# Kernel optimization log

Measured on AMD Instinct MI355X. Metric: run time of the kernel, lower is better.

The kernel has to match this reference:

```python
import jax, jax.numpy as jnp
import numpy as np


def _resize1d(x, axis, out_size):
    """Bilinear resize along one axis, align_corners=False (PyTorch semantics,
    no antialias). x: any shape; interpolates along `axis` to out_size."""
    in_size = x.shape[axis]
    src = (jnp.arange(out_size, dtype=jnp.float32) + 0.5) * (in_size / out_size) - 0.5
    src = jnp.clip(src, 0.0, in_size - 1)
    i0 = jnp.floor(src).astype(jnp.int32)
    i1 = jnp.minimum(i0 + 1, in_size - 1)
    w = (src - i0.astype(jnp.float32))
    x0 = jnp.take(x, i0, axis=axis)
    x1 = jnp.take(x, i1, axis=axis)
    shape = [1] * x.ndim
    shape[axis] = out_size
    w = w.reshape(shape)
    return x0 * (1.0 - w) + x1 * w


def bilinear_resize(x, h_out, w_out):
    """x: (..., H, W) -> (..., h_out, w_out), bilinear align_corners=False."""
    x = _resize1d(x, x.ndim - 2, h_out)
    x = _resize1d(x, x.ndim - 1, w_out)
    return x


def _deform_corr_single(f1, f2, off):
    """f1, f2: (C, H, W); off: (2, H, W) with off[0]=dx, off[1]=dy.
    Bilinearly sample f2 at (x+dx, y+dy) with zero padding outside, then
    channel dot-product with f1 -> (H, W)."""
    C, H, W = f1.shape
    ys, xs = jnp.meshgrid(jnp.arange(H, dtype=jnp.float32),
                          jnp.arange(W, dtype=jnp.float32), indexing='ij')
    sx = xs + off[0]
    sy = ys + off[1]
    x0 = jnp.floor(sx)
    y0 = jnp.floor(sy)
    x1 = x0 + 1.0
    y1 = y0 + 1.0
    wx1 = sx - x0
    wy1 = sy - y0
    wx0 = 1.0 - wx1
    wy0 = 1.0 - wy1

    def corner(yc, xc, w):
        valid = (xc >= 0) & (xc <= W - 1) & (yc >= 0) & (yc <= H - 1)
        xi = jnp.clip(xc, 0, W - 1).astype(jnp.int32)
        yi = jnp.clip(yc, 0, H - 1).astype(jnp.int32)
        vals = f2[:, yi, xi]  # (C, H, W) gather
        return vals * (w * valid.astype(f2.dtype))[None, :, :]

    sampled = (corner(y0, x0, wy0 * wx0) + corner(y0, x1, wy0 * wx1)
               + corner(y1, x0, wy1 * wx0) + corner(y1, x1, wy1 * wx1))
    return jnp.sum(f1 * sampled, axis=0)  # (H, W)


_deform_corr = jax.vmap(_deform_corr_single)  # batched over B

SCALES = [0, 1, 2]


def setup_inputs() -> dict:
    key = jax.random.key(0)
    k1, k2, k3 = jax.random.split(key, 3)
    B, C, H, W = 4, 128, 256, 256
    feat1 = jax.random.normal(k1, (B, C, H, W), dtype=jnp.float32)
    feat2 = jax.random.normal(k2, (B, C, H, W), dtype=jnp.float32)
    # offsets in a few-pixel range, as typical for deformable flow offsets
    offsets = jax.random.normal(k3, (B, 2 * len(SCALES), H, W), dtype=jnp.float32) * 4.0
    return {"feat1": feat1, "feat2": feat2, "offsets": offsets}


def reference(feat1, feat2, offsets):
    B, C, H, W = feat1.shape
    corrs = []
    for i, scale in enumerate(SCALES):
        off = offsets[:, 2 * i:2 * i + 2]
        if scale > 0:
            hs, ws = H // (2 ** scale), W // (2 ** scale)
            f1 = bilinear_resize(feat1, hs, ws)
            f2 = bilinear_resize(feat2, hs, ws)
            off = bilinear_resize(off, hs, ws) / (2.0 ** scale)
        else:
            f1, f2 = feat1, feat2
        corr = _deform_corr(f1, f2, off)  # (B, hs, ws)
        if scale > 0:
            corr = bilinear_resize(corr, H, W)
        corrs.append(corr)
    return jnp.stack(corrs, axis=1)  # (B, S, H, W)
```

## Files before the change

### kernel.cpp

```cpp
#include <hip/hip_runtime.h>

#define HH 256
#define WW 256
#define NB 4
#define NC 128
#define HW (HH * WW)

#define LADDR(p, c) (((p) << 7) + ((c) ^ ((((p) & 15)) << 1)))

__device__ __forceinline__ float blo(unsigned int u) { return __uint_as_float(u << 16); }
__device__ __forceinline__ float bhi(unsigned int u) { return __uint_as_float(u & 0xffff0000u); }
__device__ __forceinline__ unsigned int bf16_rne(float f) {
    unsigned int u = __float_as_uint(f);
    return (u + 0x7fffu + ((u >> 16) & 1u)) >> 16;
}
__device__ __forceinline__ unsigned int pack_bf16(float a, float b) {
    return bf16_rne(a) | (bf16_rne(b) << 16);
}
union U4 { uint4 v; unsigned int w[4]; };

__global__ __launch_bounds__(256) void prep3_kernel(
        const float* __restrict__ feat1, const float* __restrict__ feat2,
        unsigned int* __restrict__ s0f1, unsigned int* __restrict__ s0f2,
        unsigned int* __restrict__ d1f1, unsigned int* __restrict__ d1f2,
        unsigned int* __restrict__ d2f1, unsigned int* __restrict__ d2f2) {
    __shared__ float lds[64 * 128];

    int z = blockIdx.z;
    int b = z & 3;
    const float* src = (z < 4 ? feat1 : feat2) + (size_t)b * NC * HW;
    unsigned int* s0 = (z < 4 ? s0f1 : s0f2);
    unsigned int* d1 = (z < 4 ? d1f1 : d1f2);
    unsigned int* d2 = (z < 4 ? d2f1 : d2f2);

    int tid = threadIdx.x;
    int bx = blockIdx.x;
    int by = blockIdx.y;
    int x0 = bx * 16, y0 = by * 4;

    {
        int cband = tid >> 4;
        int f4 = tid & 15;
        int py = f4 >> 2, px4 = f4 & 3;
        const float* lp = src + (size_t)(y0 + py) * WW + x0 + px4 * 4;
        int pbase = py * 16 + px4 * 4;
#pragma unroll
        for (int it = 0; it < 8; ++it) {
            int c = it * 16 + cband;
            float4 v = *(const float4*)(lp + (size_t)c * HW);
            lds[LADDR(pbase + 0, c)] = v.x;
            lds[LADDR(pbase + 1, c)] = v.y;
            lds[LADDR(pbase + 2, c)] = v.z;
            lds[LADDR(pbase + 3, c)] = v.w;
        }
    }
    __syncthreads();

    int c8 = tid & 15;

    {
        int pq = tid >> 4;
#pragma unroll
        for (int it = 0; it < 4; ++it) {
            int p = it * 16 + pq;
            U4 u;
#pragma unroll
            for (int j = 0; j < 4; ++j) {
                float2 v = *(const float2*)&lds[LADDR(p, c8 * 8 + 2 * j)];
                u.w[j] = pack_bf16(v.x, v.y);
            }
            size_t pix = ((size_t)(b * HH + y0 + it) * WW + (x0 + pq));
            *(uint4*)(s0 + pix * 64 + c8 * 4) = u.v;
        }
    }

    {
        int dp = tid >> 4;
        int qy = dp >> 3, qx = dp & 7;
        int p00 = (2 * qy) * 16 + 2 * qx;
        U4 u;
#pragma unroll
        for (int j = 0; j < 4; ++j) {
            int ch = c8 * 8 + 2 * j;
            float2 a0 = *(const float2*)&lds[LADDR(p00,      ch)];
            float2 a1 = *(const float2*)&lds[LADDR(p00 + 1,  ch)];
            float2 a2 = *(const float2*)&lds[LADDR(p00 + 16, ch)];
            float2 a3 = *(const float2*)&lds[LADDR(p00 + 17, ch)];
            u.w[j] = pack_bf16(0.25f * (a0.x + a1.x + a2.x + a3.x),
                               0.25f * (a0.y + a1.y + a2.y + a3.y));
        }
        size_t pix = ((size_t)(b * 128 + by * 2 + qy) * 128 + (bx * 8 + qx));
        *(uint4*)(d1 + pix * 64 + c8 * 4) = u.v;
    }

    if (tid < 64) {
        int dp = tid >> 4;
        int p00 = 16 + 4 * dp + 1;
        U4 u;
#pragma unroll
        for (int j = 0; j < 4; ++j) {
            int ch = c8 * 8 + 2 * j;
            float2 a0 = *(const float2*)&lds[LADDR(p00,      ch)];
            float2 a1 = *(const float2*)&lds[LADDR(p00 + 1,  ch)];
            float2 a2 = *(const float2*)&lds[LADDR(p00 + 16, ch)];
            float2 a3 = *(const float2*)&lds[LADDR(p00 + 17, ch)];
            u.w[j] = pack_bf16(0.25f * (a0.x + a1.x + a2.x + a3.x),
                               0.25f * (a0.y + a1.y + a2.y + a3.y));
        }
        size_t pix = ((size_t)(b * 64 + by) * 64 + (bx * 4 + dp));
        *(uint4*)(d2 + pix * 64 + c8 * 4) = u.v;
    }
}

template <int SCALE>
__global__ void corr_hwc(const unsigned int* __restrict__ f1,
                         const unsigned int* __restrict__ f2,
                         const float* __restrict__ offs,
                         float* __restrict__ out) {
    constexpr int S = (SCALE == 0) ? 256 : (SCALE == 1 ? 128 : 64);
    constexpr int LOGS = (SCALE == 0) ? 8 : (SCALE == 1 ? 7 : 6);
    int tid = threadIdx.x;
    int lane = tid & 15;
    int pix = blockIdx.x * 16 + (tid >> 4);
    int b = pix >> (2 * LOGS);
    int p = pix & (S * S - 1);
    int y = p >> LOGS;
    int x = p & (S - 1);

    const float* offx = offs + ((size_t)b * 6 + 2 * SCALE) * (HH * WW);
    const float* offy = offx + HH * WW;
    float dx, dy;
    if constexpr (SCALE == 0) {
        dx = offx[y * WW + x];
        dy = offy[y * WW + x];
    } else if constexpr (SCALE == 1) {
        const float* px = offx + (2 * y) * WW + 2 * x;
        const float* py = offy + (2 * y) * WW + 2 * x;
        dx = 0.125f * (px[0] + px[1] + px[WW] + px[WW + 1]);
        dy = 0.125f * (py[0] + py[1] + py[WW] + py[WW + 1]);
    } else {
        const float* px = offx + (4 * y + 1) * WW + 4 * x + 1;
        const float* py = offy + (4 * y + 1) * WW + 4 * x + 1;
        dx = 0.0625f * (px[0] + px[1] + px[WW] + px[WW + 1]);
        dy = 0.0625f * (py[0] + py[1] + py[WW] + py[WW + 1]);
    }

    float sx = (float)x + dx;
    float sy = (float)y + dy;
    float x0f = floorf(sx), y0f = floorf(sy);
    float wx1 = sx - x0f, wy1 = sy - y0f;
    float wx0 = 1.0f - wx1, wy0 = 1.0f - wy1;
    int x0 = (int)x0f, y0 = (int)y0f;
    int x1 = x0 + 1, y1 = y0 + 1;
    bool vx0 = (x0 >= 0) & (x0 < S);
    bool vx1 = (x1 >= 0) & (x1 < S);
    bool vy0 = (y0 >= 0) & (y0 < S);
    bool vy1 = (y1 >= 0) & (y1 < S);
    float w00 = wy0 * wx0 * (float)(vy0 & vx0);
    float w01 = wy0 * wx1 * (float)(vy0 & vx1);
    float w10 = wy1 * wx0 * (float)(vy1 & vx0);
    float w11 = wy1 * wx1 * (float)(vy1 & vx1);
    int cx0 = min(max(x0, 0), S - 1), cx1 = min(max(x1, 0), S - 1);
    int cy0 = min(max(y0, 0), S - 1), cy1 = min(max(y1, 0), S - 1);
    size_t pb = (size_t)b << (2 * LOGS);
    size_t i00 = pb + (cy0 << LOGS) + cx0, i01 = pb + (cy0 << LOGS) + cx1;
    size_t i10 = pb + (cy1 << LOGS) + cx0, i11 = pb + (cy1 << LOGS) + cx1;

    int lo = lane * 4;
    U4 a, c00, c01, c10, c11;
    a.v   = *(const uint4*)(f1 + ((size_t)pix << 6) + lo);
    c00.v = *(const uint4*)(f2 + (i00 << 6) + lo);
    c01.v = *(const uint4*)(f2 + (i01 << 6) + lo);
    c10.v = *(const uint4*)(f2 + (i10 << 6) + lo);
    c11.v = *(const uint4*)(f2 + (i11 << 6) + lo);

    float acc = 0.0f;
#pragma unroll
    for (int j = 0; j < 4; ++j) {
        float s_lo = w00 * blo(c00.w[j]) + w01 * blo(c01.w[j]) + w10 * blo(c10.w[j]) + w11 * blo(c11.w[j]);
        float s_hi = w00 * bhi(c00.w[j]) + w01 * bhi(c01.w[j]) + w10 * bhi(c10.w[j]) + w11 * bhi(c11.w[j]);
        acc = fmaf(blo(a.w[j]), s_lo, acc);
        acc = fmaf(bhi(a.w[j]), s_hi, acc);
    }
    acc += __shfl_xor(acc, 8);
    acc += __shfl_xor(acc, 4);
    acc += __shfl_xor(acc, 2);
    acc += __shfl_xor(acc, 1);

    if (lane == 0) {
        if constexpr (SCALE == 0) {
            out[((size_t)b * 3) * (HH * WW) + p] = acc;
        } else {
            out[(size_t)b * (S * S) + p] = acc;
        }
    }
}

template <int SCALE>
__global__ void up_kernel(const float* __restrict__ corr, float* __restrict__ out) {
    constexpr int S = (SCALE == 1) ? 128 : 64;
    constexpr float R = (float)S / 256.0f;
    int idx = blockIdx.x * blockDim.x + threadIdx.x;
    if (idx >= NB * HH * WW) return;
    int x = idx & 255;
    int t = idx >> 8;
    int y = t & 255;
    int b = t >> 8;
    float srcx = fminf(fmaxf(((float)x + 0.5f) * R - 0.5f, 0.0f), (float)(S - 1));
    float srcy = fminf(fmaxf(((float)y + 0.5f) * R - 0.5f, 0.0f), (float)(S - 1));
    int x0 = (int)srcx;
    int y0 = (int)srcy;
    int x1 = min(x0 + 1, S - 1), y1 = min(y0 + 1, S - 1);
    float wx = srcx - (float)x0, wy = srcy - (float)y0;
    const float* cp = corr + (size_t)b * (S * S);
    float v0 = cp[y0 * S + x0] * (1.0f - wx) + cp[y0 * S + x1] * wx;
    float v1 = cp[y1 * S + x0] * (1.0f - wx) + cp[y1 * S + x1] * wx;
    out[((size_t)b * 3 + SCALE) * (HH * WW) + y * WW + x] = (1.0f - wy) * v0 + wy * v1;
}

extern "C" void kernel_launch(void* const* d_in, const int* in_sizes, int n_in,
                              void* d_out, int out_size, void* d_ws, size_t ws_size,
                              hipStream_t stream) {
    const float* feat1 = (const float*)d_in[0];
    const float* feat2 = (const float*)d_in[1];
    const float* offs  = (const float*)d_in[2];
    float* out = (float*)d_out;

    const size_t n_s0 = (size_t)NB * HH * WW * 64;
    const size_t n_d1 = (size_t)NB * 128 * 128 * 64;
    const size_t n_d2 = (size_t)NB * 64 * 64 * 64;
    const size_t n_c1 = (size_t)NB * 128 * 128;
    const size_t n_c2 = (size_t)NB * 64 * 64;
    const size_t need = (2 * (n_s0 + n_d1 + n_d2) + n_c1 + n_c2) * 4;
    if (ws_size < need) return;

    unsigned int* ws = (unsigned int*)d_ws;
    unsigned int* s0f1 = ws;
    unsigned int* s0f2 = s0f1 + n_s0;
    unsigned int* d1f1 = s0f2 + n_s0;
    unsigned int* d1f2 = d1f1 + n_d1;
    unsigned int* d2f1 = d1f2 + n_d1;
    unsigned int* d2f2 = d2f1 + n_d2;
    float* corr1 = (float*)(d2f2 + n_d2);
    float* corr2 = corr1 + n_c1;

    prep3_kernel<<<dim3(16, 64, 8), 256, 0, stream>>>(feat1, feat2, s0f1, s0f2,
                                                      d1f1, d1f2, d2f1, d2f2);

    corr_hwc<0><<<NB * 65536 / 16, 256, 0, stream>>>(s0f1, s0f2, offs, out);
    corr_hwc<1><<<NB * 16384 / 16, 256, 0, stream>>>(d1f1, d1f2, offs, corr1);
    corr_hwc<2><<<NB * 4096 / 16, 256, 0, stream>>>(d2f1, d2f2, offs, corr2);

    up_kernel<1><<<(NB * HH * WW + 255) / 256, 256, 0, stream>>>(corr1, out);
    up_kernel<2><<<(NB * HH * WW + 255) / 256, 256, 0, stream>>>(corr2, out);
}
```

Baseline: 159.6 us.

## Split prep into row-wise bf16 transpose and separate downsample kernels from bf16 HWC

Replaces the fused prep kernel with a transpose kernel that packs channel pairs to bf16 before writing to LDS, using full 128-pixel rows for wider coalesced reads. The 2x and 4x downsamples move into separate kernels that read the bf16 HWC scale-0 buffer instead of fp32 LDS. This halves the LDS footprint per element and simplifies the transpose, but adds two launches and extra global reads of the scale-0 buffer. Averaging already-rounded bf16 values changes rounding slightly.

```diff
diff --git a/kernel.cpp b/kernel.cpp
--- a/kernel.cpp
+++ b/kernel.cpp
@@ -6,8 +6,6 @@
 #define NC 128
 #define HW (HH * WW)
 
-#define LADDR(p, c) (((p) << 7) + ((c) ^ ((((p) & 15)) << 1)))
-
 __device__ __forceinline__ float blo(unsigned int u) { return __uint_as_float(u << 16); }
 __device__ __forceinline__ float bhi(unsigned int u) { return __uint_as_float(u & 0xffff0000u); }
 __device__ __forceinline__ unsigned int bf16_rne(float f) {
@@ -19,97 +17,89 @@
 }
 union U4 { uint4 v; unsigned int w[4]; };
 
-__global__ __launch_bounds__(256) void prep3_kernel(
+__global__ __launch_bounds__(256) void prep5_kernel(
         const float* __restrict__ feat1, const float* __restrict__ feat2,
-        unsigned int* __restrict__ s0f1, unsigned int* __restrict__ s0f2,
-        unsigned int* __restrict__ d1f1, unsigned int* __restrict__ d1f2,
-        unsigned int* __restrict__ d2f1, unsigned int* __restrict__ d2f2) {
-    __shared__ float lds[64 * 128];
+        unsigned int* __restrict__ s0f1, unsigned int* __restrict__ s0f2) {
+    __shared__ unsigned int lds[64 * 128];
 
     int z = blockIdx.z;
     int b = z & 3;
     const float* src = (z < 4 ? feat1 : feat2) + (size_t)b * NC * HW;
     unsigned int* s0 = (z < 4 ? s0f1 : s0f2);
-    unsigned int* d1 = (z < 4 ? d1f1 : d1f2);
-    unsigned int* d2 = (z < 4 ? d2f1 : d2f2);
-
+
+    int y  = blockIdx.y;
+    int bx = blockIdx.x;
     int tid = threadIdx.x;
-    int bx = blockIdx.x;
-    int by = blockIdx.y;
-    int x0 = bx * 16, y0 = by * 4;
-
-    {
-        int cband = tid >> 4;
-        int f4 = tid & 15;
-        int py = f4 >> 2, px4 = f4 & 3;
-        const float* lp = src + (size_t)(y0 + py) * WW + x0 + px4 * 4;
-        int pbase = py * 16 + px4 * 4;
-#pragma unroll
-        for (int it = 0; it < 8; ++it) {
-            int c = it * 16 + cband;
-            float4 v = *(const float4*)(lp + (size_t)c * HW);
-            lds[LADDR(pbase + 0, c)] = v.x;
-            lds[LADDR(pbase + 1, c)] = v.y;
-            lds[LADDR(pbase + 2, c)] = v.z;
-            lds[LADDR(pbase + 3, c)] = v.w;
-        }
+    int w = tid >> 6;
+    int l = tid & 63;
+    int lp = l & 31;
+    int ch = l >> 5;
+
+    const float* rowp = src + (size_t)y * WW + bx * 128 + 4 * lp;
+
+#pragma unroll
+    for (int it = 0; it < 8; ++it) {
+        int cp = it * 8 + w * 2 + ch;
+        const float* pa = rowp + (size_t)(2 * cp) * HW;
+        float4 v0 = *(const float4*)pa;
+        float4 v1 = *(const float4*)(pa + HW);
+        unsigned int h = ((cp >> 2) & 7) << 2;
+        U4 u;
+        u.w[0] = pack_bf16(v0.x, v1.x);
+        u.w[1] = pack_bf16(v0.y, v1.y);
+        u.w[2] = pack_bf16(v0.z, v1.z);
+        u.w[3] = pack_bf16(v0.w, v1.w);
+        *(uint4*)&lds[cp * 128 + ((4 * lp) ^ h)] = u.v;
     }
     __syncthreads();
 
+    int c8 = l & 15;
+    int pq = l >> 4;
+    int hr = (c8 & 7) << 2;
+#pragma unroll
+    for (int it = 0; it < 8; ++it) {
+        int p = w * 32 + it * 4 + pq;
+        int ps = p ^ hr;
+        U4 u;
+        u.w[0] = lds[(c8 * 4 + 0) * 128 + ps];
+        u.w[1] = lds[(c8 * 4 + 1) * 128 + ps];
+        u.w[2] = lds[(c8 * 4 + 2) * 128 + ps];
+        u.w[3] = lds[(c8 * 4 + 3) * 128 + ps];
+        size_t pix = ((size_t)(b * HH + y) * WW + bx * 128 + p);
+        *(uint4*)(s0 + pix * 64 + c8 * 4) = u.v;
+    }
+}
+
+template <int SC>
+__global__ __launch_bounds__(256) void ds_hwc(
+        const unsigned int* __restrict__ s0f1, const unsigned int* __restrict__ s0f2,
+        unsigned int* __restrict__ df1, unsigned int* __restrict__ df2) {
+    constexpr int S = (SC == 1) ? 128 : 64;
+    int z = blockIdx.y;
+    int b = z & 3;
+    const unsigned int* s0 = (z < 4 ? s0f1 : s0f2) + ((size_t)b * HH * WW) * 64;
+    unsigned int* d = (z < 4 ? df1 : df2) + ((size_t)b * S * S) * 64;
+
+    int tid = blockIdx.x * 256 + threadIdx.x;
     int c8 = tid & 15;
-
-    {
-        int pq = tid >> 4;
-#pragma unroll
-        for (int it = 0; it < 4; ++it) {
-            int p = it * 16 + pq;
-            U4 u;
-#pragma unroll
-            for (int j = 0; j < 4; ++j) {
-                float2 v = *(const float2*)&lds[LADDR(p, c8 * 8 + 2 * j)];
-                u.w[j] = pack_bf16(v.x, v.y);
-            }
-            size_t pix = ((size_t)(b * HH + y0 + it) * WW + (x0 + pq));
-            *(uint4*)(s0 + pix * 64 + c8 * 4) = u.v;
-        }
-    }
-
-    {
-        int dp = tid >> 4;
-        int qy = dp >> 3, qx = dp & 7;
-        int p00 = (2 * qy) * 16 + 2 * qx;
-        U4 u;
-#pragma unroll
-        for (int j = 0; j < 4; ++j) {
-            int ch = c8 * 8 + 2 * j;
-            float2 a0 = *(const float2*)&lds[LADDR(p00,      ch)];
-            float2 a1 = *(const float2*)&lds[LADDR(p00 + 1,  ch)];
-            float2 a2 = *(const float2*)&lds[LADDR(p00 + 16, ch)];
-            float2 a3 = *(const float2*)&lds[LADDR(p00 + 17, ch)];
-            u.w[j] = pack_bf16(0.25f * (a0.x + a1.x + a2.x + a3.x),
-                               0.25f * (a0.y + a1.y + a2.y + a3.y));
-        }
-        size_t pix = ((size_t)(b * 128 + by * 2 + qy) * 128 + (bx * 8 + qx));
-        *(uint4*)(d1 + pix * 64 + c8 * 4) = u.v;
-    }
-
-    if (tid < 64) {
-        int dp = tid >> 4;
-        int p00 = 16 + 4 * dp + 1;
-        U4 u;
-#pragma unroll
-        for (int j = 0; j < 4; ++j) {
-            int ch = c8 * 8 + 2 * j;
-            float2 a0 = *(const float2*)&lds[LADDR(p00,      ch)];
-            float2 a1 = *(const float2*)&lds[LADDR(p00 + 1,  ch)];
-            float2 a2 = *(const float2*)&lds[LADDR(p00 + 16, ch)];
-            float2 a3 = *(const float2*)&lds[LADDR(p00 + 17, ch)];
-            u.w[j] = pack_bf16(0.25f * (a0.x + a1.x + a2.x + a3.x),
-                               0.25f * (a0.y + a1.y + a2.y + a3.y));
-        }
-        size_t pix = ((size_t)(b * 64 + by) * 64 + (bx * 4 + dp));
-        *(uint4*)(d2 + pix * 64 + c8 * 4) = u.v;
-    }
+    int p = tid >> 4;
+    int yo = p / S, xo = p % S;
+    int yi = (SC == 1) ? 2 * yo : 4 * yo + 1;
+    int xi = (SC == 1) ? 2 * xo : 4 * xo + 1;
+
+    const unsigned int* p00 = s0 + ((size_t)(yi * WW + xi)) * 64 + c8 * 4;
+    U4 a, bb, c, dd, o;
+    a.v  = *(const uint4*)p00;
+    bb.v = *(const uint4*)(p00 + 64);
+    c.v  = *(const uint4*)(p00 + WW * 64);
+    dd.v = *(const uint4*)(p00 + WW * 64 + 64);
+#pragma unroll
+    for (int j = 0; j < 4; ++j) {
+        float lo = blo(a.w[j]) + blo(bb.w[j]) + blo(c.w[j]) + blo(dd.w[j]);
+        float hi = bhi(a.w[j]) + bhi(bb.w[j]) + bhi(c.w[j]) + bhi(dd.w[j]);
+        o.w[j] = pack_bf16(0.25f * lo, 0.25f * hi);
+    }
+    *(uint4*)(d + (size_t)p * 64 + c8 * 4) = o.v;
 }
 
 template <int SCALE>
@@ -244,8 +234,10 @@
     float* corr1 = (float*)(d2f2 + n_d2);
     float* corr2 = corr1 + n_c1;
 
-    prep3_kernel<<<dim3(16, 64, 8), 256, 0, stream>>>(feat1, feat2, s0f1, s0f2,
-                                                      d1f1, d1f2, d2f1, d2f2);
+    prep5_kernel<<<dim3(2, 256, 8), 256, 0, stream>>>(feat1, feat2, s0f1, s0f2);
+
+    ds_hwc<1><<<dim3(1024, 8), 256, 0, stream>>>(s0f1, s0f2, d1f1, d1f2);
+    ds_hwc<2><<<dim3(256, 8), 256, 0, stream>>>(s0f1, s0f2, d2f1, d2f2);
 
     corr_hwc<0><<<NB * 65536 / 16, 256, 0, stream>>>(s0f1, s0f2, offs, out);
     corr_hwc<1><<<NB * 16384 / 16, 256, 0, stream>>>(d1f1, d1f2, offs, corr1);
```

Result: faster. 145.3 us (-9.0%).
